# Performance work log

Measured on AMD Instinct MI355X. Metric: run time of the kernel, lower is better.

Reference implementation:

```python
import jax, jax.numpy as jnp
import numpy as np

N_BINS = 256
TAU = 0.01
EPS = 1e-10


def setup_inputs() -> dict:
    key = jax.random.key(0)
    x = jax.random.uniform(key, (4, 1, 512, 512), dtype=jnp.float32)
    return {"x": x}


def reference(x):
    B, _, H, W = x.shape
    bins = jnp.linspace(0.0, 1.0, N_BINS, dtype=x.dtype)  # (n_bins,)
    xf = x.reshape(B, H * W, 1)                            # (B, HW, 1)
    diff = xf - bins[None, None, :]                        # (B, HW, n_bins)
    weights = jnp.exp(-jnp.square(diff) / (2.0 * TAU ** 2))
    # soft histogram over pixels, normalized per image
    histogram = weights.sum(axis=1)                        # (B, n_bins)
    histogram = histogram / (histogram.sum(axis=1, keepdims=True) + EPS)
    cdf = jnp.cumsum(histogram, axis=1)                    # (B, n_bins)
    cdf_min = cdf[:, 0:1]
    cdf_normalized = (cdf - cdf_min) / (1.0 - cdf_min + EPS)
    # per-pixel soft lookup into the normalized CDF
    weights_norm = weights / (weights.sum(axis=-1, keepdims=True) + EPS)
    equalized_flat = (weights_norm * cdf_normalized[:, None, :]).sum(axis=-1)  # (B, HW)
    return equalized_flat.reshape(B, 1, H, W)
```

## Files before the change

kernel.cpp:

```cpp
#include <hip/hip_runtime.h>
#include <math.h>

#define N_BINS 256
#define TAU 0.01f
#define EPS 1e-10f
#define HW (512*512)
#define Q 4081
#define QSTRIDE 4096
#define MWIN 208
#define WTAB (2*MWIN+1)
#define WPADN 432
#define NP 27
#define CFP_STRIDE 289
#define NPART 64
#define BMAX 4

__device__ __align__(64) unsigned int g_l1[32 * 16];
__device__ __align__(64) unsigned int g_l2v = 0u;
__device__ __align__(64) unsigned int g_gen = 0u;
__device__ __align__(16) float g_partT[BMAX * NPART * N_BINS];

__global__ __launch_bounds__(512) void fused_equalize_kernel(const float* __restrict__ x,
                                                             float* __restrict__ out,
                                                             int nblk, int ngrp) {
    __shared__ union {
        float cfp[16 * CFP_STRIDE];
        float Tl[QSTRIDE];
    } A;
    __shared__ union {
        unsigned int lh[QSTRIDE];
        float ph[256 * 17];
        struct {
            float red2[512];
            float wsum[4];
            float h0s;
        } p2;
    } Bu;
    __shared__ float wtE[WPADN];
    __shared__ float cdfnp[288];
    __shared__ float onesp[288];

    const int b    = blockIdx.y;
    const int s    = blockIdx.x;
    const int bid  = b * NPART + s;
    const int tid  = threadIdx.x;
    const int r    = tid & 15;
    const int t    = tid >> 4;
    const int lane = tid & 63;

    unsigned int mygen = 0u;
    if (tid == 0)
        mygen = __hip_atomic_load(&g_gen, __ATOMIC_RELAXED, __HIP_MEMORY_SCOPE_AGENT);

    for (int i = tid; i < QSTRIDE; i += 512) Bu.lh[i] = 0u;
    for (int i = tid; i < 16 * CFP_STRIDE; i += 512) A.cfp[i] = 0.f;
    for (int i = tid; i < WPADN; i += 512) {
        const float d = (float)(i - MWIN) * (1.0f / 4080.f);
        wtE[i] = (i < WTAB) ? __expf(-d * d * (1.0f / (2.0f * TAU * TAU))) : 0.f;
    }
    for (int i = tid; i < 288; i += 512) {
        cdfnp[i] = 0.f;
        onesp[i] = (i >= 13 && i < 269) ? 1.f : 0.f;
    }

    const float4* xb = (const float4*)(x + (size_t)b * HW + (size_t)s * 4096);
    float4 px[2];
    px[0] = xb[tid];
    px[1] = xb[512 + tid];
    __syncthreads();

#pragma unroll
    for (int i = 0; i < 2; ++i) {
        const float4 v = px[i];
        int q0 = __float2int_rn(v.x * 4080.f);
        int q1 = __float2int_rn(v.y * 4080.f);
        int q2 = __float2int_rn(v.z * 4080.f);
        int q3 = __float2int_rn(v.w * 4080.f);
        q0 = min(max(q0, 0), Q - 1); q1 = min(max(q1, 0), Q - 1);
        q2 = min(max(q2, 0), Q - 1); q3 = min(max(q3, 0), Q - 1);
        atomicAdd(&Bu.lh[q0], 1u); atomicAdd(&Bu.lh[q1], 1u);
        atomicAdd(&Bu.lh[q2], 1u); atomicAdd(&Bu.lh[q3], 1u);
    }
    __syncthreads();

#pragma unroll
    for (int k = 0; k < 8; ++k) {
        const int q = k * 512 + tid;
        A.cfp[(q & 15) * CFP_STRIDE + (q >> 4) + 13] = (float)Bu.lh[q];
    }
    __syncthreads();

    {
        float creg[34];
        const float* cbase = &A.cfp[r * CFP_STRIDE + 8 * t];
#pragma unroll
        for (int k = 0; k < 34; ++k) creg[k] = cbase[k];
        float acc[8];
#pragma unroll
        for (int uu = 0; uu < 8; ++uu) acc[uu] = 0.f;
#pragma unroll
        for (int p = 0; p < NP; ++p) {
            const float w = wtE[16 * p + r];
#pragma unroll
            for (int uu = 0; uu < 8; ++uu) acc[uu] += w * creg[uu + p];
        }
#pragma unroll
        for (int uu = 0; uu < 8; ++uu) Bu.ph[(8 * t + uu) * 17 + r] = acc[uu];
    }
    __syncthreads();

    if (tid < N_BINS) {
        float hv = 0.f;
#pragma unroll
        for (int rr = 0; rr < 16; ++rr) hv += Bu.ph[tid * 17 + rr];
        __hip_atomic_store(&g_partT[(size_t)bid * N_BINS + tid], hv,
                           __ATOMIC_RELAXED, __HIP_MEMORY_SCOPE_AGENT);
    }

    __syncthreads();
    if (tid == 0) {
        bool master = false;
        unsigned int* c1 = &g_l1[(bid >> 3) * 16];
        const unsigned int p1 = __hip_atomic_fetch_add(c1, 1u, __ATOMIC_RELAXED,
                                                       __HIP_MEMORY_SCOPE_AGENT);
        if (p1 == 7u) {
            __hip_atomic_store(c1, 0u, __ATOMIC_RELAXED, __HIP_MEMORY_SCOPE_AGENT);
            const unsigned int p2 = __hip_atomic_fetch_add(&g_l2v, 1u, __ATOMIC_RELAXED,
                                                           __HIP_MEMORY_SCOPE_AGENT);
            if (p2 == (unsigned int)(ngrp - 1)) {
                __hip_atomic_store(&g_l2v, 0u, __ATOMIC_RELAXED, __HIP_MEMORY_SCOPE_AGENT);
                __hip_atomic_fetch_add(&g_gen, 1u, __ATOMIC_RELAXED,
                                       __HIP_MEMORY_SCOPE_AGENT);
                master = true;
            }
        }
        if (!master) {
            while (__hip_atomic_load(&g_gen, __ATOMIC_RELAXED,
                                     __HIP_MEMORY_SCOPE_AGENT) == mygen) {
                __builtin_amdgcn_s_sleep(1);
            }
        }
        (void)__hip_atomic_load(&g_gen, __ATOMIC_ACQUIRE, __HIP_MEMORY_SCOPE_AGENT);
    }
    __syncthreads();

    {
        const int bin  = tid & 255;
        const int half = tid >> 8;
        float* pb = &g_partT[(size_t)b * NPART * N_BINS + (size_t)half * 32 * N_BINS + bin];
        float hv2 = 0.f;
#pragma unroll
        for (int rr = 0; rr < 32; ++rr)
            hv2 += __hip_atomic_load(pb + (size_t)rr * N_BINS, __ATOMIC_RELAXED,
                                     __HIP_MEMORY_SCOPE_AGENT);
        Bu.p2.red2[half * 256 + bin] = hv2;
    }
    __syncthreads();

    float val = 0.f, hv = 0.f;
    if (tid < N_BINS) {
        hv = Bu.p2.red2[tid] + Bu.p2.red2[256 + tid];
        val = hv;
#pragma unroll
        for (int d = 1; d < 64; d <<= 1) {
            const float n = __shfl_up(val, (unsigned)d, 64);
            if (lane >= d) val += n;
        }
        if (lane == 63) Bu.p2.wsum[tid >> 6] = val;
        if (tid == 0) Bu.p2.h0s = hv;
    }
    __syncthreads();
    if (tid < N_BINS) {
        float prefix = 0.f, total = 0.f;
#pragma unroll
        for (int w2 = 0; w2 < 4; ++w2) {
            const float ws = Bu.p2.wsum[w2];
            if (w2 < (tid >> 6)) prefix += ws;
            total += ws;
        }
        val += prefix;
        const float inv  = 1.0f / (total + EPS);
        const float cdf0 = Bu.p2.h0s * inv;
        cdfnp[tid + 13] = (val * inv - cdf0) / (1.0f - cdf0 + EPS);
    }
    __syncthreads();

    {
        float creg[34], oreg[34];
        const int base = 8 * t;
#pragma unroll
        for (int k = 0; k < 34; ++k) { creg[k] = cdfnp[base + k]; oreg[k] = onesp[base + k]; }
        float acc[8], sw[8];
#pragma unroll
        for (int uu = 0; uu < 8; ++uu) { acc[uu] = 0.f; sw[uu] = 0.f; }
#pragma unroll
        for (int p = 0; p < NP; ++p) {
            const float w = wtE[16 * p + r];
#pragma unroll
            for (int uu = 0; uu < 8; ++uu) {
                const int k = uu - p + 26;
                acc[uu] += w * creg[k];
                sw[uu]  += w * oreg[k];
            }
        }
#pragma unroll
        for (int uu = 0; uu < 8; ++uu)
            A.Tl[16 * (8 * t + uu) + r] = acc[uu] / (sw[uu] + EPS);
    }
    __syncthreads();

    float4* ob = (float4*)(out + (size_t)b * HW + (size_t)s * 4096);
#pragma unroll
    for (int i = 0; i < 2; ++i) {
        const float4 v = px[i];
        const float vv[4] = {v.x, v.y, v.z, v.w};
        float res[4];
#pragma unroll
        for (int k2 = 0; k2 < 4; ++k2) {
            const float u = vv[k2] * 4080.f;
            int q = (int)u;
            q = min(max(q, 0), Q - 2);
            const float frac = u - (float)q;
            const float t0 = A.Tl[q], t1 = A.Tl[q + 1];
            res[k2] = fmaf(frac, t1 - t0, t0);
        }
        ob[i * 512 + tid] = make_float4(res[0], res[1], res[2], res[3]);
    }
}

extern "C" void kernel_launch(void* const* d_in, const int* in_sizes, int n_in,
                              void* d_out, int out_size, void* d_ws, size_t ws_size,
                              hipStream_t stream) {
    const float* x = (const float*)d_in[0];
    float* out     = (float*)d_out;
    const int B    = in_sizes[0] / HW;
    const int nblk = NPART * B;
    const int ngrp = nblk / 8;

    fused_equalize_kernel<<<dim3(NPART, B), 512, 0, stream>>>(x, out, nblk, ngrp);
}
```

Measured before the change: 63.85 us.

## Use per-image barriers and atomic global histogram accumulation with parity buffers

The single grid-wide two-level barrier becomes an independent barrier per image, so each image's blocks wait only for their own partials. Instead of writing 64 per-block partial histograms and having every block re-read and reduce them after the barrier, blocks float-atomically add their partials into a padded global histogram per image. That histogram is double-buffered by generation parity, with block 0 clearing the other buffer for the next launch. This cuts post-barrier global reads and barrier scope, at the cost of contended float atomics and nondeterministic summation order.

```diff
diff --git a/kernel.cpp b/kernel.cpp
--- a/kernel.cpp
+++ b/kernel.cpp
@@ -14,15 +14,15 @@
 #define CFP_STRIDE 289
 #define NPART 64
 #define BMAX 4
-
-__device__ __align__(64) unsigned int g_l1[32 * 16];
-__device__ __align__(64) unsigned int g_l2v = 0u;
-__device__ __align__(64) unsigned int g_gen = 0u;
-__device__ __align__(16) float g_partT[BMAX * NPART * N_BINS];
+#define HSTRIDE 16
+
+__device__ __align__(64) unsigned int g_c1[BMAX * 8 * 16];
+__device__ __align__(64) unsigned int g_c2[BMAX * 16];
+__device__ __align__(64) unsigned int g_gen[BMAX * 16];
+__device__ __align__(16) float g_hist[2][BMAX][N_BINS * HSTRIDE];
 
 __global__ __launch_bounds__(512) void fused_equalize_kernel(const float* __restrict__ x,
-                                                             float* __restrict__ out,
-                                                             int nblk, int ngrp) {
+                                                             float* __restrict__ out) {
     __shared__ union {
         float cfp[16 * CFP_STRIDE];
         float Tl[QSTRIDE];
@@ -30,27 +30,22 @@
     __shared__ union {
         unsigned int lh[QSTRIDE];
         float ph[256 * 17];
-        struct {
-            float red2[512];
-            float wsum[4];
-            float h0s;
-        } p2;
+        struct { float wsum[4]; float h0s; } p2;
     } Bu;
     __shared__ float wtE[WPADN];
     __shared__ float cdfnp[288];
     __shared__ float onesp[288];
+    __shared__ unsigned int bgen;
 
     const int b    = blockIdx.y;
     const int s    = blockIdx.x;
-    const int bid  = b * NPART + s;
     const int tid  = threadIdx.x;
     const int r    = tid & 15;
     const int t    = tid >> 4;
     const int lane = tid & 63;
 
-    unsigned int mygen = 0u;
     if (tid == 0)
-        mygen = __hip_atomic_load(&g_gen, __ATOMIC_RELAXED, __HIP_MEMORY_SCOPE_AGENT);
+        bgen = __hip_atomic_load(&g_gen[b * 16], __ATOMIC_RELAXED, __HIP_MEMORY_SCOPE_AGENT);
 
     for (int i = tid; i < QSTRIDE; i += 512) Bu.lh[i] = 0u;
     for (int i = tid; i < 16 * CFP_STRIDE; i += 512) A.cfp[i] = 0.f;
@@ -68,6 +63,13 @@
     px[0] = xb[tid];
     px[1] = xb[512 + tid];
     __syncthreads();
+
+    const unsigned int mygen = bgen;
+    const int par = (int)(mygen & 1u);
+
+    if (s == 0 && tid < N_BINS)
+        __hip_atomic_store(&g_hist[par ^ 1][b][tid * HSTRIDE], 0.f,
+                           __ATOMIC_RELAXED, __HIP_MEMORY_SCOPE_AGENT);
 
 #pragma unroll
     for (int i = 0; i < 2; ++i) {
@@ -113,53 +115,42 @@
         float hv = 0.f;
 #pragma unroll
         for (int rr = 0; rr < 16; ++rr) hv += Bu.ph[tid * 17 + rr];
-        __hip_atomic_store(&g_partT[(size_t)bid * N_BINS + tid], hv,
-                           __ATOMIC_RELAXED, __HIP_MEMORY_SCOPE_AGENT);
+        atomicAdd(&g_hist[par][b][tid * HSTRIDE], hv);
     }
 
     __syncthreads();
     if (tid == 0) {
         bool master = false;
-        unsigned int* c1 = &g_l1[(bid >> 3) * 16];
+        unsigned int* c1 = &g_c1[(b * 8 + (s >> 3)) * 16];
         const unsigned int p1 = __hip_atomic_fetch_add(c1, 1u, __ATOMIC_RELAXED,
                                                        __HIP_MEMORY_SCOPE_AGENT);
         if (p1 == 7u) {
             __hip_atomic_store(c1, 0u, __ATOMIC_RELAXED, __HIP_MEMORY_SCOPE_AGENT);
-            const unsigned int p2 = __hip_atomic_fetch_add(&g_l2v, 1u, __ATOMIC_RELAXED,
+            const unsigned int p2 = __hip_atomic_fetch_add(&g_c2[b * 16], 1u,
+                                                           __ATOMIC_RELAXED,
                                                            __HIP_MEMORY_SCOPE_AGENT);
-            if (p2 == (unsigned int)(ngrp - 1)) {
-                __hip_atomic_store(&g_l2v, 0u, __ATOMIC_RELAXED, __HIP_MEMORY_SCOPE_AGENT);
-                __hip_atomic_fetch_add(&g_gen, 1u, __ATOMIC_RELAXED,
+            if (p2 == 7u) {
+                __hip_atomic_store(&g_c2[b * 16], 0u, __ATOMIC_RELAXED,
+                                   __HIP_MEMORY_SCOPE_AGENT);
+                __hip_atomic_fetch_add(&g_gen[b * 16], 1u, __ATOMIC_RELAXED,
                                        __HIP_MEMORY_SCOPE_AGENT);
                 master = true;
             }
         }
         if (!master) {
-            while (__hip_atomic_load(&g_gen, __ATOMIC_RELAXED,
+            while (__hip_atomic_load(&g_gen[b * 16], __ATOMIC_RELAXED,
                                      __HIP_MEMORY_SCOPE_AGENT) == mygen) {
                 __builtin_amdgcn_s_sleep(1);
             }
         }
-        (void)__hip_atomic_load(&g_gen, __ATOMIC_ACQUIRE, __HIP_MEMORY_SCOPE_AGENT);
-    }
-    __syncthreads();
-
-    {
-        const int bin  = tid & 255;
-        const int half = tid >> 8;
-        float* pb = &g_partT[(size_t)b * NPART * N_BINS + (size_t)half * 32 * N_BINS + bin];
-        float hv2 = 0.f;
-#pragma unroll
-        for (int rr = 0; rr < 32; ++rr)
-            hv2 += __hip_atomic_load(pb + (size_t)rr * N_BINS, __ATOMIC_RELAXED,
-                                     __HIP_MEMORY_SCOPE_AGENT);
-        Bu.p2.red2[half * 256 + bin] = hv2;
+        (void)__hip_atomic_load(&g_gen[b * 16], __ATOMIC_ACQUIRE, __HIP_MEMORY_SCOPE_AGENT);
     }
     __syncthreads();
 
     float val = 0.f, hv = 0.f;
     if (tid < N_BINS) {
-        hv = Bu.p2.red2[tid] + Bu.p2.red2[256 + tid];
+        hv = __hip_atomic_load(&g_hist[par][b][tid * HSTRIDE], __ATOMIC_RELAXED,
+                               __HIP_MEMORY_SCOPE_AGENT);
         val = hv;
 #pragma unroll
         for (int d = 1; d < 64; d <<= 1) {
@@ -234,8 +225,6 @@
     const float* x = (const float*)d_in[0];
     float* out     = (float*)d_out;
     const int B    = in_sizes[0] / HW;
-    const int nblk = NPART * B;
-    const int ngrp = nblk / 8;
-
-    fused_equalize_kernel<<<dim3(NPART, B), 512, 0, stream>>>(x, out, nblk, ngrp);
+
+    fused_equalize_kernel<<<dim3(NPART, B), 512, 0, stream>>>(x, out);
 }
```

Measured after the change: 68.36 us. 7.1% more time.
